# Performance work log

Measured on AMD Instinct MI355X. Metric: run time of the kernel, lower is better.

The kernel has to match this reference:

```python
import jax, jax.numpy as jnp
import numpy as np

SCALE = 2
PAD = 4
EPS = 1e-5
K = 5
N, C, H, W = 4, 64, 128, 128


def _splits(a, s):
    # (..., W, H) -> (..., W/s, H/s, s*s), block decimation matching torch view/permute
    *lead, Wd, Hd = a.shape
    b = a.reshape(*lead, s, Wd // s, s, Hd // s)
    nl = len(lead)
    b = jnp.transpose(b, tuple(range(nl)) + (nl + 1, nl + 3, nl, nl + 2))
    return b.reshape(*lead, Wd // s, Hd // s, s * s)


def _p2o(psf, Hs, Ws):
    # PSF -> OTF: zero-pad, roll to center at origin, FFT
    kh, kw = psf.shape[-2], psf.shape[-1]
    otf = jnp.zeros(psf.shape[:-2] + (Hs, Ws), psf.dtype).at[..., :kh, :kw].set(psf)
    otf = jnp.roll(otf, (-(kh // 2), -(kw // 2)), axis=(-2, -1))
    return jnp.fft.fftn(otf, axes=(-2, -1))


def _upsample(x, s):
    # s-fold zero-filling upsampler (S^T y)
    n, c, h, w = x.shape
    return jnp.zeros((n, c, h * s, w * s), x.dtype).at[..., ::s, ::s].set(x)


def setup_inputs() -> dict:
    key = jax.random.key(0)
    kx, kw_, _ = jax.random.split(key, 3)
    x = jax.random.normal(kx, (N, C, H, W), dtype=jnp.float32)
    w_raw = jax.random.normal(kw_, (1, C, K, K), dtype=jnp.float32)
    weight = jax.nn.softmax(w_raw.reshape(1, C, -1), axis=-1).reshape(1, C, K, K)
    bias = jnp.zeros((1, C, 1, 1), dtype=jnp.float32)
    return {"x": x, "weight": weight, "bias": bias}


def reference(x, weight, bias):
    s = SCALE
    xp = jnp.pad(x, ((0, 0), (0, 0), (PAD, PAD), (PAD, PAD)), mode="wrap")  # circular
    biaseps = jax.nn.sigmoid(bias - 9.0) + EPS  # (1,C,1,1)
    _, _, h, w = xp.shape
    STy = _upsample(xp, s)  # zero-filled upsample
    # nearest-neighbor interpolate by integer factor s
    xn = jnp.repeat(jnp.repeat(xp, s, axis=-2), s, axis=-1)
    FB = _p2o(weight, h * s, w * s)           # (1,C,hs,ws) complex
    FBC = jnp.conj(FB)
    F2B = jnp.abs(FB) ** 2                     # real
    FBFy = FBC * jnp.fft.fftn(STy, axes=(-2, -1))
    FR = FBFy + jnp.fft.fftn(biaseps * xn, axes=(-2, -1))
    x1 = FB * FR
    FBR = jnp.mean(_splits(x1, s), axis=-1)    # (N,C,h,w) complex
    invW = jnp.mean(_splits(F2B, s), axis=-1)  # (1,C,h,w) real
    invWBR = FBR / (invW + biaseps)
    FCBinvWBR = FBC * jnp.tile(invWBR, (1, 1, s, s))
    FX = (FR - FCBinvWBR) / biaseps
    out = jnp.real(jnp.fft.ifftn(FX, axes=(-2, -1)))
    out = out[..., PAD * s:-PAD * s, PAD * s:-PAD * s]
    return out
```

## Files before the change

### kernel.cpp

```cpp
#include <hip/hip_runtime.h>
#include <math.h>


#define MDIM 136
#define RSC  70
#define HC   69
#define PLANE_HALF (MDIM*HC)
#define NPLANES 256
#define LDS_CPLX (MDIM*RSC + MDIM)
#define PI_D 3.14159265358979323846

__device__ __forceinline__ int slot136(int k) { return 17*(k & 7) + (k >> 3); }
__device__ __forceinline__ int slot68(int k)  { return 17*(k & 3) + (k >> 2); }

template<int DIR>
__device__ __forceinline__ void dft17(float2* __restrict__ z, int base, int stride)
{
    constexpr float C17[9] = {1.f, 0.93247223f, 0.73900892f, 0.44573836f,
                              0.09226836f, -0.27366299f, -0.60263464f,
                              -0.85021714f, -0.98297310f};
    constexpr float S17[9] = {0.f, 0.36124167f, 0.67369564f, 0.89516329f,
                              0.99573418f, 0.96182564f, 0.79801723f,
                              0.52643216f, 0.18374952f};
    constexpr float d = (DIR > 0) ? 1.f : -1.f;
    float xr[17], xi[17];
#pragma unroll
    for (int n = 0; n < 17; n++) {
        float2 v = z[base + n*stride];
        xr[n] = v.x; xi[n] = v.y;
    }
    float ar[8], ai[8], br[8], bi[8];
#pragma unroll
    for (int n = 1; n <= 8; n++) {
        ar[n-1] = xr[n] + xr[17-n];  ai[n-1] = xi[n] + xi[17-n];
        br[n-1] = xr[n] - xr[17-n];  bi[n-1] = xi[n] - xi[17-n];
    }
    float s0r = xr[0], s0i = xi[0];
#pragma unroll
    for (int n = 0; n < 8; n++) { s0r += ar[n]; s0i += ai[n]; }
    z[base] = make_float2(s0r, s0i);
#pragma unroll
    for (int k = 1; k <= 8; k++) {
        float Pr = xr[0], Pi = xi[0], Qr = 0.f, Qi = 0.f;
#pragma unroll
        for (int n = 1; n <= 8; n++) {
            int m = (k*n) % 17;
            float cc = (m <= 8) ? C17[m] : C17[17-m];
            float ss = (m <= 8) ? S17[m] : -S17[17-m];
            Pr = fmaf(ar[n-1], cc, Pr);
            Pi = fmaf(ai[n-1], cc, Pi);
            Qr = fmaf(br[n-1], ss, Qr);
            Qi = fmaf(bi[n-1], ss, Qi);
        }
        z[base + k*stride]      = make_float2(Pr - d*Qi, Pi + d*Qr);
        z[base + (17-k)*stride] = make_float2(Pr + d*Qi, Pi - d*Qr);
    }
}

template<int DIR>
__device__ void fft136_cols(float2* __restrict__ z, const float2* __restrict__ lut,
                            int ncols, int tid, int nth)
{
    constexpr float d = (DIR > 0) ? 1.0f : -1.0f;
    constexpr float C707 = 0.70710678118654752f;
    for (int e = tid; e < ncols*17; e += nth) {
        int c  = e / 17;
        int n2 = e - c*17;
        float xr[8], xi[8];
#pragma unroll
        for (int n1 = 0; n1 < 8; n1++) {
            float2 v = z[(17*n1 + n2)*RSC + c];
            xr[n1] = v.x; xi[n1] = v.y;
        }
        float e0r = xr[0]+xr[4], e0i = xi[0]+xi[4];
        float e1r = xr[0]-xr[4], e1i = xi[0]-xi[4];
        float o0r = xr[2]+xr[6], o0i = xi[2]+xi[6];
        float o1r = xr[2]-xr[6], o1i = xi[2]-xi[6];
        float E0r = e0r+o0r, E0i = e0i+o0i;
        float E2r = e0r-o0r, E2i = e0i-o0i;
        float E1r = e1r - d*o1i, E1i = e1i + d*o1r;
        float E3r = e1r + d*o1i, E3i = e1i - d*o1r;
        float f0r = xr[1]+xr[5], f0i = xi[1]+xi[5];
        float f1r = xr[1]-xr[5], f1i = xi[1]-xi[5];
        float h0r = xr[3]+xr[7], h0i = xi[3]+xi[7];
        float h1r = xr[3]-xr[7], h1i = xi[3]-xi[7];
        float O0r = f0r+h0r, O0i = f0i+h0i;
        float O2r = f0r-h0r, O2i = f0i-h0i;
        float O1r = f1r - d*h1i, O1i = f1i + d*h1r;
        float O3r = f1r + d*h1i, O3i = f1i - d*h1r;
        float t1r =  C707*(O1r - d*O1i), t1i = C707*(O1i + d*O1r);
        float t2r = -d*O2i,              t2i = d*O2r;
        float t3r = -C707*(O3r + d*O3i), t3i = C707*(d*O3r - O3i);
        float Xr[8], Xi[8];
        Xr[0]=E0r+O0r; Xi[0]=E0i+O0i;  Xr[4]=E0r-O0r; Xi[4]=E0i-O0i;
        Xr[1]=E1r+t1r; Xi[1]=E1i+t1i;  Xr[5]=E1r-t1r; Xi[5]=E1i-t1i;
        Xr[2]=E2r+t2r; Xi[2]=E2i+t2i;  Xr[6]=E2r-t2r; Xi[6]=E2i-t2i;
        Xr[3]=E3r+t3r; Xi[3]=E3i+t3i;  Xr[7]=E3r-t3r; Xi[7]=E3i-t3i;
        float2 w = lut[n2];
        float wr = w.x, wi = w.y;
        float cr = 1.f, ci = 0.f;
#pragma unroll
        for (int k1 = 0; k1 < 8; k1++) {
            int a = (17*k1 + n2)*RSC + c;
            z[a] = make_float2(Xr[k1]*cr - Xi[k1]*ci, Xr[k1]*ci + Xi[k1]*cr);
            float ncr = cr*wr - ci*wi;
            ci = cr*wi + ci*wr; cr = ncr;
        }
    }
    __syncthreads();
    for (int e = tid; e < ncols*8; e += nth) {
        int c  = e >> 3;
        int k1 = e & 7;
        dft17<DIR>(z, 17*k1*RSC + c, RSC);
    }
    __syncthreads();
}

template<int DIR>
__device__ void ct68_rows(float2* __restrict__ z, const float2* __restrict__ lut,
                          int tid, int nth)
{
    constexpr float d = (DIR > 0) ? 1.0f : -1.0f;
    for (int e = tid; e < MDIM*17; e += nth) {
        int row = e / 17;
        int n2  = e - row*17;
        int base = row*RSC;
        float xr[4], xi[4];
#pragma unroll
        for (int n1 = 0; n1 < 4; n1++) {
            float2 v = z[base + 17*n1 + n2];
            xr[n1] = v.x; xi[n1] = v.y;
        }
        float t0r = xr[0]+xr[2], t0i = xi[0]+xi[2];
        float t1r = xr[0]-xr[2], t1i = xi[0]-xi[2];
        float t2r = xr[1]+xr[3], t2i = xi[1]+xi[3];
        float t3r = xr[1]-xr[3], t3i = xi[1]-xi[3];
        float Xr[4], Xi[4];
        Xr[0] = t0r+t2r;      Xi[0] = t0i+t2i;
        Xr[2] = t0r-t2r;      Xi[2] = t0i-t2i;
        Xr[1] = t1r - d*t3i;  Xi[1] = t1i + d*t3r;
        Xr[3] = t1r + d*t3i;  Xi[3] = t1i - d*t3r;
        float2 w = lut[2*n2];
        float wr = w.x, wi = w.y;
        float cr = 1.f, ci = 0.f;
#pragma unroll
        for (int k1 = 0; k1 < 4; k1++) {
            int a = base + 17*k1 + n2;
            z[a] = make_float2(Xr[k1]*cr - Xi[k1]*ci, Xr[k1]*ci + Xi[k1]*cr);
            float ncr = cr*wr - ci*wi;
            ci = cr*wi + ci*wr; cr = ncr;
        }
    }
    __syncthreads();
    for (int e = tid; e < MDIM*4; e += nth) {
        int row = e >> 2;
        int k1  = e & 3;
        dft17<DIR>(z, row*RSC + 17*k1, 1);
    }
    __syncthreads();
}

__global__ __launch_bounds__(1024, 8) void fwd_kernel(const float* __restrict__ x,
                                                      float2* __restrict__ Xhat)
{
    extern __shared__ float2 zsm[];
    float2* z   = zsm;
    float2* lut = zsm + MDIM*RSC;
    const int tid = threadIdx.x, nth = blockDim.x;

    for (int t = tid; t < MDIM; t += nth) {
        double s, c; sincos(-2.0*PI_D*(double)t/136.0, &s, &c);
        lut[t] = make_float2((float)c, (float)s);
    }
    const float* xp = x + (size_t)blockIdx.x * (128*128);
    for (int e = tid; e < MDIM*68; e += nth) {
        int i = e / 68, n = e - i*68;
        int si = (i + 124) & 127;
        int j0 = (2*n + 124) & 127;
        z[i*RSC + n] = *reinterpret_cast<const float2*>(xp + si*128 + j0);
    }
    __syncthreads();
    ct68_rows<-1>(z, lut, tid, nth);
    for (int e = tid; e < MDIM*35; e += nth) {
        int row = e / 35, k = e - row*35;
        int base = row*RSC;
        int sa = slot68(k);
        float2 Za = z[base+sa];
        float Zar = Za.x, Zai = Za.y;
        float Zbr, Zbi; int sb;
        if (k == 0) { Zbr = Zar; Zbi = Zai; sb = 68; }
        else {
            int kk = 68-k; sb = slot68(kk);
            float2 Zb = z[base+sb]; Zbr = Zb.x; Zbi = Zb.y;
        }
        float2 w = lut[k];
        float wc = w.x, ws = w.y;
        float Er = 0.5f*(Zar + Zbr), Ei = 0.5f*(Zai - Zbi);
        float Dr = 0.5f*(Zar - Zbr), Di = 0.5f*(Zai + Zbi);
        float Tr = wc*Dr - ws*Di, Ti = wc*Di + ws*Dr;
        z[base+sa] = make_float2(Er + Ti, Ei - Tr);
        float E2r = Er,  E2i = -Ei;
        float D2r = -Dr, D2i = Di;
        float w2c = -wc, w2s = ws;
        float T2r = w2c*D2r - w2s*D2i, T2i = w2c*D2i + w2s*D2r;
        z[base+sb] = make_float2(E2r + T2i, E2i - T2r);
    }
    __syncthreads();
    fft136_cols<-1>(z, lut, HC, tid, nth);
    float2* outp = Xhat + (size_t)blockIdx.x * PLANE_HALF;
    for (int e = tid; e < PLANE_HALF; e += nth) {
        int g1 = e / HC, g2 = e - g1*HC;
        int cq = (g2 == 68) ? 68 : slot68(g2);
        outp[e] = z[slot136(g1)*RSC + cq];
    }
}

__global__ void prep_kernel(const float* __restrict__ weight,
                            const float* __restrict__ bias,
                            float2* __restrict__ Abuf)
{
    __shared__ double tabc[272], tabs[272];
    for (int t = threadIdx.x; t < 272; t += blockDim.x) {
        double s, c; sincos(-2.0*PI_D*(double)t/272.0, &s, &c);
        tabc[t] = c; tabs[t] = s;
    }
    __syncthreads();

    const int c     = blockIdx.x >> 3;
    const int chunk = blockIdx.x & 7;
    const float* wp = weight + c*25;
    double w[25];
#pragma unroll
    for (int i = 0; i < 25; i++) w[i] = (double)wp[i];
    const double r = 1.0/(1.0 + exp(9.0 - (double)bias[c])) + 1e-5;

    const int e_lo = chunk * 1173;
    const int e_hi = e_lo + 1173;
    for (int e = e_lo + (int)threadIdx.x; e < e_hi; e += blockDim.x) {
        int g1 = e / HC, g2 = e - g1*HC;
        double c1 = tabc[g1], s1 = tabs[g1];
        double c2 = tabc[g2], s2 = tabs[g2];
        double e1r[5], e1i[5], e2r[5], e2i[5];
        e1r[2]=1.0; e1i[2]=0.0; e1r[3]=c1; e1i[3]=s1;
        e1r[4]=c1*c1-s1*s1; e1i[4]=2.0*c1*s1;
        e1r[1]=c1; e1i[1]=-s1; e1r[0]=e1r[4]; e1i[0]=-e1i[4];
        e2r[2]=1.0; e2i[2]=0.0; e2r[3]=c2; e2i[3]=s2;
        e2r[4]=c2*c2-s2*s2; e2i[4]=2.0*c2*s2;
        e2r[1]=c2; e2i[1]=-s2; e2r[0]=e2r[4]; e2i[0]=-e2i[4];

        double R0r[5],R0i[5],R1r[5],R1i[5];
#pragma unroll
        for (int a = 0; a < 5; a++) {
            double r0r=0,r0i=0,r1r=0,r1i=0;
#pragma unroll
            for (int b = 0; b < 5; b++) {
                double wv = w[a*5+b];
                double pr = wv*e2r[b], pi = wv*e2i[b];
                r0r += pr; r0i += pi;
                if (b & 1) { r1r -= pr; r1i -= pi; } else { r1r += pr; r1i += pi; }
            }
            R0r[a]=r0r; R0i[a]=r0i; R1r[a]=r1r; R1i[a]=r1i;
        }
        double FBr[2][2], FBi[2][2];
#pragma unroll
        for (int a1 = 0; a1 < 2; a1++)
#pragma unroll
            for (int b1 = 0; b1 < 2; b1++) {
                double fr=0, fi=0;
#pragma unroll
                for (int a = 0; a < 5; a++) {
                    double er = e1r[a], ei = e1i[a];
                    if (a1 && (a & 1)) { er = -er; ei = -ei; }
                    double Rr = b1 ? R1r[a] : R0r[a];
                    double Ri = b1 ? R1i[a] : R0i[a];
                    fr += er*Rr - ei*Ri;
                    fi += er*Ri + ei*Rr;
                }
                FBr[a1][b1]=fr; FBi[a1][b1]=fi;
            }
        double ur[2]={1.0+c1, 1.0-c1}, ui[2]={s1, -s1};
        double vr[2]={1.0+c2, 1.0-c2}, vi[2]={s2, -s2};
        double Br_[2][2], Bi_[2][2];
#pragma unroll
        for (int a1 = 0; a1 < 2; a1++)
#pragma unroll
            for (int b1 = 0; b1 < 2; b1++) {
                Br_[a1][b1] = ur[a1]*vr[b1] - ui[a1]*vi[b1];
                Bi_[a1][b1] = ur[a1]*vi[b1] + ui[a1]*vr[b1];
            }
        double invW=0, Qr=0, Qi=0;
#pragma unroll
        for (int a1 = 0; a1 < 2; a1++)
#pragma unroll
            for (int b1 = 0; b1 < 2; b1++) {
                invW += FBr[a1][b1]*FBr[a1][b1] + FBi[a1][b1]*FBi[a1][b1];
                Qr += FBr[a1][b1]*Br_[a1][b1] - FBi[a1][b1]*Bi_[a1][b1];
                Qi += FBr[a1][b1]*Bi_[a1][b1] + FBi[a1][b1]*Br_[a1][b1];
            }
        invW *= 0.25; Qr *= 0.25; Qi *= 0.25;
        double den = 1.0/(invW + r);
        double Sr = (1.0 - Qr)*den, Si = -Qi*den;
        double Mr[2][2], Mi[2][2];
#pragma unroll
        for (int a1 = 0; a1 < 2; a1++)
#pragma unroll
            for (int b1 = 0; b1 < 2; b1++) {
                Mr[a1][b1] = Br_[a1][b1] + FBr[a1][b1]*Sr + FBi[a1][b1]*Si;
                Mi[a1][b1] = Bi_[a1][b1] + FBr[a1][b1]*Si - FBi[a1][b1]*Sr;
            }
        const double scale = 1.0/73984.0;
#pragma unroll
        for (int uu = 0; uu < 2; uu++)
#pragma unroll
            for (int vv = 0; vv < 2; vv++) {
                double sr=0, si=0;
#pragma unroll
                for (int a1 = 0; a1 < 2; a1++)
#pragma unroll
                    for (int b1 = 0; b1 < 2; b1++) {
                        if ((a1*uu + b1*vv) & 1) { sr -= Mr[a1][b1]; si -= Mi[a1][b1]; }
                        else                     { sr += Mr[a1][b1]; si += Mi[a1][b1]; }
                    }
                int t = g1*uu + g2*vv;
                double pc = tabc[t], ps = -tabs[t];
                float2 outv;
                outv.x = (float)((pc*sr - ps*si)*scale);
                outv.y = (float)((pc*si + ps*sr)*scale);
                Abuf[((size_t)(c*4 + uu*2 + vv))*PLANE_HALF + e] = outv;
            }
    }
}

__global__ __launch_bounds__(1024, 8) void inv_kernel(const float2* __restrict__ Xhat,
                                                      const float2* __restrict__ Abuf,
                                                      float* __restrict__ out)
{
    extern __shared__ float2 zsm[];
    float2* z   = zsm;
    float2* lut = zsm + MDIM*RSC;
    const int tid = threadIdx.x, nth = blockDim.x;

    for (int t = tid; t < MDIM; t += nth) {
        double s, c; sincos(2.0*PI_D*(double)t/136.0, &s, &c);
        lut[t] = make_float2((float)c, (float)s);
    }
    const int p  = blockIdx.x;
    const int u  = p & 1;
    const int v  = (p >> 3) & 1;
    const int nc = ((p >> 4) << 2) | ((p >> 1) & 3);
    const int c  = nc & 63;
    const float2* Xp = Xhat + (size_t)nc * PLANE_HALF;
    const float2* Ap = Abuf + (size_t)(c*4 + u*2 + v) * PLANE_HALF;

    for (int e = tid; e < PLANE_HALF; e += nth) {
        int g1 = e / HC, g2 = e - g1*HC;
        float2 xv = Xp[e], av = Ap[e];
        z[g1*RSC + g2] = make_float2(av.x*xv.x - av.y*xv.y,
                                     av.x*xv.y + av.y*xv.x);
    }
    __syncthreads();
    fft136_cols<1>(z, lut, HC, tid, nth);
    for (int e = tid; e < MDIM*35; e += nth) {
        int row = e / 35, k = e - row*35;
        int base = row*RSC;
        float2 Ta = z[base+k];
        float2 Tb = z[base+68-k];
        float Tar = Ta.x, Tai = Ta.y;
        float Tbr = Tb.x, Tbi = Tb.y;
        float Sr = Tar + Tbr, Si = Tai - Tbi;
        float Dr = Tar - Tbr, Di = Tai + Tbi;
        float2 w = lut[k];
        float wc = w.x, ws = w.y;
        float Or = wc*Dr - ws*Di, Oi = wc*Di + ws*Dr;
        z[base+k] = make_float2(Sr - Oi, Si + Or);
        if (k >= 1 && k <= 33) {
            float S2r = Tbr + Tar, S2i = Tbi - Tai;
            float D2r = Tbr - Tar, D2i = Tbi + Tai;
            float w2c = -wc, w2s = ws;
            float O2r = w2c*D2r - w2s*D2i, O2i = w2c*D2i + w2s*D2r;
            z[base+68-k] = make_float2(S2r - O2i, S2i + O2r);
        }
    }
    __syncthreads();
    ct68_rows<1>(z, lut, tid, nth);
    float* op = out + (size_t)nc * (256*256);
    for (int e = tid; e < 128*64; e += nth) {
        int y1 = 4 + (e >> 6);
        int m  = 2 + (e & 63);
        float2 wv = z[slot136(y1)*RSC + slot68(m)];
        int o1 = 2*y1 + u - 8;
        op[o1*256 + 4*m + v - 8] = wv.x;
        op[o1*256 + 4*m + v - 6] = wv.y;
    }
}

extern "C" void kernel_launch(void* const* d_in, const int* in_sizes, int n_in,
                              void* d_out, int out_size, void* d_ws, size_t ws_size,
                              hipStream_t stream)
{
    const float* x      = (const float*)d_in[0];
    const float* weight = (const float*)d_in[1];
    const float* bias   = (const float*)d_in[2];
    float* out = (float*)d_out;

    float2* Xhat = (float2*)d_ws;
    float2* Abuf = Xhat + (size_t)NPLANES * PLANE_HALF;

    const size_t lds_bytes = (size_t)LDS_CPLX * sizeof(float2);
    (void)hipFuncSetAttribute((const void*)fwd_kernel,
                              hipFuncAttributeMaxDynamicSharedMemorySize, (int)lds_bytes);
    (void)hipFuncSetAttribute((const void*)inv_kernel,
                              hipFuncAttributeMaxDynamicSharedMemorySize, (int)lds_bytes);

    prep_kernel<<<512, 256, 0, stream>>>(weight, bias, Abuf);
    fwd_kernel<<<NPLANES, 1024, lds_bytes, stream>>>(x, Xhat);
    inv_kernel<<<NPLANES*4, 1024, lds_bytes, stream>>>(Xhat, Abuf, out);
}
```

Baseline: 151.2 us.

## Fuse final DFT17 stages with global stores and merge c2r pack into radix-4 pass

The final radix-17 DFT pass of each FFT now writes its outputs straight to global memory, with the index permutation built in. This removes a shared-memory round trip, a barrier and the separate gather/scatter loop. In the inverse kernel, the complex-to-real untangling step is merged with the first radix-4 row stage. The change also strength-reduces index math (no divides inside loops, using a fixed 1024 threads), reads twiddles from the LUT directly instead of recurrence multiplies, and computes the LUT with float sincosf instead of double. The global stores become strided or scattered, which may hurt coalescing, and float twiddles reduce accuracy slightly.

Measured after the change: 166.8 us. +10.4%, slower.

```diff
diff --git a/kernel.cpp b/kernel.cpp
--- a/kernel.cpp
+++ b/kernel.cpp
@@ -9,12 +9,12 @@
 #define NPLANES 256
 #define LDS_CPLX (MDIM*RSC + MDIM)
 #define PI_D 3.14159265358979323846
-
-__device__ __forceinline__ int slot136(int k) { return 17*(k & 7) + (k >> 3); }
+#define NTH 1024
+
 __device__ __forceinline__ int slot68(int k)  { return 17*(k & 3) + (k >> 2); }
 
-template<int DIR>
-__device__ __forceinline__ void dft17(float2* __restrict__ z, int base, int stride)
+template<int DIR, class F>
+__device__ __forceinline__ void dft17_sink(float2* z, int base, int stride, F f)
 {
     constexpr float C17[9] = {1.f, 0.93247223f, 0.73900892f, 0.44573836f,
                               0.09226836f, -0.27366299f, -0.60263464f,
@@ -38,7 +38,7 @@
     float s0r = xr[0], s0i = xi[0];
 #pragma unroll
     for (int n = 0; n < 8; n++) { s0r += ar[n]; s0i += ai[n]; }
-    z[base] = make_float2(s0r, s0i);
+    f(0, s0r, s0i);
 #pragma unroll
     for (int k = 1; k <= 8; k++) {
         float Pr = xr[0], Pi = xi[0], Qr = 0.f, Qi = 0.f;
@@ -52,20 +52,39 @@
             Qr = fmaf(br[n-1], ss, Qr);
             Qi = fmaf(bi[n-1], ss, Qi);
         }
-        z[base + k*stride]      = make_float2(Pr - d*Qi, Pi + d*Qr);
-        z[base + (17-k)*stride] = make_float2(Pr + d*Qi, Pi - d*Qr);
+        f(k,    Pr - d*Qi, Pi + d*Qr);
+        f(17-k, Pr + d*Qi, Pi - d*Qr);
     }
 }
 
 template<int DIR>
-__device__ void fft136_cols(float2* __restrict__ z, const float2* __restrict__ lut,
-                            int ncols, int tid, int nth)
+__device__ __forceinline__ void radix4_tw(float2* z, const float2* lut, int base, int n2,
+                                          float2 Z0, float2 Z1, float2 Z2, float2 Z3)
+{
+    constexpr float d = (DIR > 0) ? 1.0f : -1.0f;
+    float t0r = Z0.x+Z2.x, t0i = Z0.y+Z2.y;
+    float t1r = Z0.x-Z2.x, t1i = Z0.y-Z2.y;
+    float t2r = Z1.x+Z3.x, t2i = Z1.y+Z3.y;
+    float t3r = Z1.x-Z3.x, t3i = Z1.y-Z3.y;
+    float X0r = t0r+t2r,     X0i = t0i+t2i;
+    float X2r = t0r-t2r,     X2i = t0i-t2i;
+    float X1r = t1r - d*t3i, X1i = t1i + d*t3r;
+    float X3r = t1r + d*t3i, X3i = t1i - d*t3r;
+    z[base + n2] = make_float2(X0r, X0i);
+    float2 w1 = lut[2*n2], w2 = lut[4*n2], w3 = lut[6*n2];
+    z[base + 17 + n2] = make_float2(X1r*w1.x - X1i*w1.y, X1r*w1.y + X1i*w1.x);
+    z[base + 34 + n2] = make_float2(X2r*w2.x - X2i*w2.y, X2r*w2.y + X2i*w2.x);
+    z[base + 51 + n2] = make_float2(X3r*w3.x - X3i*w3.y, X3r*w3.y + X3i*w3.x);
+}
+
+template<int DIR>
+__device__ void fft136_s1(float2* z, const float2* lut, int ncols, int tid)
 {
     constexpr float d = (DIR > 0) ? 1.0f : -1.0f;
     constexpr float C707 = 0.70710678118654752f;
-    for (int e = tid; e < ncols*17; e += nth) {
-        int c  = e / 17;
-        int n2 = e - c*17;
+    int c = tid / 17;
+    int n2 = tid - c*17;
+    for (int e = tid; e < ncols*17; e += NTH) {
         float xr[8], xi[8];
 #pragma unroll
         for (int n1 = 0; n1 < 8; n1++) {
@@ -96,68 +115,41 @@
         Xr[1]=E1r+t1r; Xi[1]=E1i+t1i;  Xr[5]=E1r-t1r; Xi[5]=E1i-t1i;
         Xr[2]=E2r+t2r; Xi[2]=E2i+t2i;  Xr[6]=E2r-t2r; Xi[6]=E2i-t2i;
         Xr[3]=E3r+t3r; Xi[3]=E3i+t3i;  Xr[7]=E3r-t3r; Xi[7]=E3i-t3i;
-        float2 w = lut[n2];
-        float wr = w.x, wi = w.y;
-        float cr = 1.f, ci = 0.f;
-#pragma unroll
-        for (int k1 = 0; k1 < 8; k1++) {
-            int a = (17*k1 + n2)*RSC + c;
-            z[a] = make_float2(Xr[k1]*cr - Xi[k1]*ci, Xr[k1]*ci + Xi[k1]*cr);
-            float ncr = cr*wr - ci*wi;
-            ci = cr*wi + ci*wr; cr = ncr;
-        }
-    }
-    __syncthreads();
-    for (int e = tid; e < ncols*8; e += nth) {
-        int c  = e >> 3;
-        int k1 = e & 7;
-        dft17<DIR>(z, 17*k1*RSC + c, RSC);
-    }
-    __syncthreads();
+        z[n2*RSC + c] = make_float2(Xr[0], Xi[0]);
+        int ti = 0;
+#pragma unroll
+        for (int k1 = 1; k1 < 8; k1++) {
+            ti += n2;
+            float2 w = lut[ti];
+            z[(17*k1 + n2)*RSC + c] = make_float2(Xr[k1]*w.x - Xi[k1]*w.y,
+                                                  Xr[k1]*w.y + Xi[k1]*w.x);
+        }
+        c += 60; n2 += 4; if (n2 >= 17) { n2 -= 17; c++; }
+    }
 }
 
 template<int DIR>
-__device__ void ct68_rows(float2* __restrict__ z, const float2* __restrict__ lut,
-                          int tid, int nth)
-{
-    constexpr float d = (DIR > 0) ? 1.0f : -1.0f;
-    for (int e = tid; e < MDIM*17; e += nth) {
-        int row = e / 17;
-        int n2  = e - row*17;
+__device__ void ct68_s1(float2* z, const float2* lut, int tid)
+{
+    int row = tid / 17;
+    int n2  = tid - row*17;
+    for (int e = tid; e < MDIM*17; e += NTH) {
         int base = row*RSC;
-        float xr[4], xi[4];
-#pragma unroll
-        for (int n1 = 0; n1 < 4; n1++) {
-            float2 v = z[base + 17*n1 + n2];
-            xr[n1] = v.x; xi[n1] = v.y;
-        }
-        float t0r = xr[0]+xr[2], t0i = xi[0]+xi[2];
-        float t1r = xr[0]-xr[2], t1i = xi[0]-xi[2];
-        float t2r = xr[1]+xr[3], t2i = xi[1]+xi[3];
-        float t3r = xr[1]-xr[3], t3i = xi[1]-xi[3];
-        float Xr[4], Xi[4];
-        Xr[0] = t0r+t2r;      Xi[0] = t0i+t2i;
-        Xr[2] = t0r-t2r;      Xi[2] = t0i-t2i;
-        Xr[1] = t1r - d*t3i;  Xi[1] = t1i + d*t3r;
-        Xr[3] = t1r + d*t3i;  Xi[3] = t1i - d*t3r;
-        float2 w = lut[2*n2];
-        float wr = w.x, wi = w.y;
-        float cr = 1.f, ci = 0.f;
-#pragma unroll
-        for (int k1 = 0; k1 < 4; k1++) {
-            int a = base + 17*k1 + n2;
-            z[a] = make_float2(Xr[k1]*cr - Xi[k1]*ci, Xr[k1]*ci + Xi[k1]*cr);
-            float ncr = cr*wr - ci*wi;
-            ci = cr*wi + ci*wr; cr = ncr;
-        }
-    }
-    __syncthreads();
-    for (int e = tid; e < MDIM*4; e += nth) {
-        int row = e >> 2;
-        int k1  = e & 3;
-        dft17<DIR>(z, row*RSC + 17*k1, 1);
-    }
-    __syncthreads();
+        float2 Z0 = z[base + n2];
+        float2 Z1 = z[base + 17 + n2];
+        float2 Z2 = z[base + 34 + n2];
+        float2 Z3 = z[base + 51 + n2];
+        radix4_tw<DIR>(z, lut, base, n2, Z0, Z1, Z2, Z3);
+        row += 60; n2 += 4; if (n2 >= 17) { n2 -= 17; row++; }
+    }
+}
+
+__device__ __forceinline__ float2 c2r_pack(float2 a, float2 b, float2 w)
+{
+    float Sr = a.x + b.x, Si = a.y - b.y;
+    float Dr = a.x - b.x, Di = a.y + b.y;
+    float Or = w.x*Dr - w.y*Di, Oi = w.x*Di + w.y*Dr;
+    return make_float2(Sr - Oi, Si + Or);
 }
 
 __global__ __launch_bounds__(1024, 8) void fwd_kernel(const float* __restrict__ x,
@@ -166,52 +158,73 @@
     extern __shared__ float2 zsm[];
     float2* z   = zsm;
     float2* lut = zsm + MDIM*RSC;
-    const int tid = threadIdx.x, nth = blockDim.x;
-
-    for (int t = tid; t < MDIM; t += nth) {
-        double s, c; sincos(-2.0*PI_D*(double)t/136.0, &s, &c);
-        lut[t] = make_float2((float)c, (float)s);
+    const int tid = threadIdx.x;
+
+    if (tid < MDIM) {
+        float s, c; sincosf(-2.0f*(float)PI_D*(float)tid/136.0f, &s, &c);
+        lut[tid] = make_float2(c, s);
     }
     const float* xp = x + (size_t)blockIdx.x * (128*128);
-    for (int e = tid; e < MDIM*68; e += nth) {
-        int i = e / 68, n = e - i*68;
-        int si = (i + 124) & 127;
-        int j0 = (2*n + 124) & 127;
-        z[i*RSC + n] = *reinterpret_cast<const float2*>(xp + si*128 + j0);
-    }
-    __syncthreads();
-    ct68_rows<-1>(z, lut, tid, nth);
-    for (int e = tid; e < MDIM*35; e += nth) {
-        int row = e / 35, k = e - row*35;
-        int base = row*RSC;
-        int sa = slot68(k);
-        float2 Za = z[base+sa];
-        float Zar = Za.x, Zai = Za.y;
-        float Zbr, Zbi; int sb;
-        if (k == 0) { Zbr = Zar; Zbi = Zai; sb = 68; }
-        else {
-            int kk = 68-k; sb = slot68(kk);
-            float2 Zb = z[base+sb]; Zbr = Zb.x; Zbi = Zb.y;
-        }
-        float2 w = lut[k];
-        float wc = w.x, ws = w.y;
-        float Er = 0.5f*(Zar + Zbr), Ei = 0.5f*(Zai - Zbi);
-        float Dr = 0.5f*(Zar - Zbr), Di = 0.5f*(Zai + Zbi);
-        float Tr = wc*Dr - ws*Di, Ti = wc*Di + ws*Dr;
-        z[base+sa] = make_float2(Er + Ti, Ei - Tr);
-        float E2r = Er,  E2i = -Ei;
-        float D2r = -Dr, D2i = Di;
-        float w2c = -wc, w2s = ws;
-        float T2r = w2c*D2r - w2s*D2i, T2i = w2c*D2i + w2s*D2r;
-        z[base+sb] = make_float2(E2r + T2i, E2i - T2r);
-    }
-    __syncthreads();
-    fft136_cols<-1>(z, lut, HC, tid, nth);
+    {
+        int i = tid / 68, n = tid - (tid/68)*68;
+        for (int e = tid; e < MDIM*68; e += NTH) {
+            int si = (i + 124) & 127;
+            int j0 = (2*n + 124) & 127;
+            z[i*RSC + n] = *reinterpret_cast<const float2*>(xp + si*128 + j0);
+            i += 15; n += 4; if (n >= 68) { n -= 68; i++; }
+        }
+    }
+    __syncthreads();
+    ct68_s1<-1>(z, lut, tid);
+    __syncthreads();
+    if (tid < MDIM*4) {
+        int row = tid >> 2, k1 = tid & 3;
+        int base = row*RSC + 17*k1;
+        dft17_sink<-1>(z, base, 1, [&](int k2, float re, float im) {
+            z[base + k2] = make_float2(re, im);
+        });
+    }
+    __syncthreads();
+    {
+        int row = tid / 35, k = tid - (tid/35)*35;
+        for (int e = tid; e < MDIM*35; e += NTH) {
+            int base = row*RSC;
+            int sa = slot68(k);
+            float2 Za = z[base+sa];
+            float Zar = Za.x, Zai = Za.y;
+            float Zbr, Zbi; int sb;
+            if (k == 0) { Zbr = Zar; Zbi = Zai; sb = 68; }
+            else {
+                int kk = 68-k; sb = slot68(kk);
+                float2 Zb = z[base+sb]; Zbr = Zb.x; Zbi = Zb.y;
+            }
+            float2 w = lut[k];
+            float wc = w.x, ws = w.y;
+            float Er = 0.5f*(Zar + Zbr), Ei = 0.5f*(Zai - Zbi);
+            float Dr = 0.5f*(Zar - Zbr), Di = 0.5f*(Zai + Zbi);
+            float Tr = wc*Dr - ws*Di, Ti = wc*Di + ws*Dr;
+            z[base+sa] = make_float2(Er + Ti, Ei - Tr);
+            float E2r = Er,  E2i = -Ei;
+            float D2r = -Dr, D2i = Di;
+            float w2c = -wc, w2s = ws;
+            float T2r = w2c*D2r - w2s*D2i, T2i = w2c*D2i + w2s*D2r;
+            z[base+sb] = make_float2(E2r + T2i, E2i - T2r);
+            row += 29; k += 9; if (k >= 35) { k -= 35; row++; }
+        }
+    }
+    __syncthreads();
+    fft136_s1<-1>(z, lut, HC, tid);
+    __syncthreads();
     float2* outp = Xhat + (size_t)blockIdx.x * PLANE_HALF;
-    for (int e = tid; e < PLANE_HALF; e += nth) {
-        int g1 = e / HC, g2 = e - g1*HC;
-        int cq = (g2 == 68) ? 68 : slot68(g2);
-        outp[e] = z[slot136(g1)*RSC + cq];
+    if (tid < HC*8) {
+        int c = tid >> 3, k1 = tid & 7;
+        int cd = (c*241) >> 12;
+        int cm = c - 17*cd;
+        int g2 = (c == 68) ? 68 : (4*cm + cd);
+        float2* op2 = outp + g2;
+        dft17_sink<-1>(z, 17*k1*RSC + c, RSC, [&](int k2, float re, float im) {
+            op2[(size_t)(k1 + 8*k2)*HC] = make_float2(re, im);
+        });
     }
 }
 
@@ -338,11 +351,11 @@
     extern __shared__ float2 zsm[];
     float2* z   = zsm;
     float2* lut = zsm + MDIM*RSC;
-    const int tid = threadIdx.x, nth = blockDim.x;
-
-    for (int t = tid; t < MDIM; t += nth) {
-        double s, c; sincos(2.0*PI_D*(double)t/136.0, &s, &c);
-        lut[t] = make_float2((float)c, (float)s);
+    const int tid = threadIdx.x;
+
+    if (tid < MDIM) {
+        float s, c; sincosf(2.0f*(float)PI_D*(float)tid/136.0f, &s, &c);
+        lut[tid] = make_float2(c, s);
     }
     const int p  = blockIdx.x;
     const int u  = p & 1;
@@ -352,45 +365,75 @@
     const float2* Xp = Xhat + (size_t)nc * PLANE_HALF;
     const float2* Ap = Abuf + (size_t)(c*4 + u*2 + v) * PLANE_HALF;
 
-    for (int e = tid; e < PLANE_HALF; e += nth) {
-        int g1 = e / HC, g2 = e - g1*HC;
-        float2 xv = Xp[e], av = Ap[e];
-        z[g1*RSC + g2] = make_float2(av.x*xv.x - av.y*xv.y,
-                                     av.x*xv.y + av.y*xv.x);
-    }
-    __syncthreads();
-    fft136_cols<1>(z, lut, HC, tid, nth);
-    for (int e = tid; e < MDIM*35; e += nth) {
-        int row = e / 35, k = e - row*35;
-        int base = row*RSC;
-        float2 Ta = z[base+k];
-        float2 Tb = z[base+68-k];
-        float Tar = Ta.x, Tai = Ta.y;
-        float Tbr = Tb.x, Tbi = Tb.y;
-        float Sr = Tar + Tbr, Si = Tai - Tbi;
-        float Dr = Tar - Tbr, Di = Tai + Tbi;
-        float2 w = lut[k];
-        float wc = w.x, ws = w.y;
-        float Or = wc*Dr - ws*Di, Oi = wc*Di + ws*Dr;
-        z[base+k] = make_float2(Sr - Oi, Si + Or);
-        if (k >= 1 && k <= 33) {
-            float S2r = Tbr + Tar, S2i = Tbi - Tai;
-            float D2r = Tbr - Tar, D2i = Tbi + Tai;
-            float w2c = -wc, w2s = ws;
-            float O2r = w2c*D2r - w2s*D2i, O2i = w2c*D2i + w2s*D2r;
-            z[base+68-k] = make_float2(S2r - O2i, S2i + O2r);
-        }
-    }
-    __syncthreads();
-    ct68_rows<1>(z, lut, tid, nth);
+    {
+        int g1 = tid / HC, g2 = tid - (tid/HC)*HC;
+        for (int e = tid; e < PLANE_HALF; e += NTH) {
+            float2 xv = Xp[e], av = Ap[e];
+            z[g1*RSC + g2] = make_float2(av.x*xv.x - av.y*xv.y,
+                                         av.x*xv.y + av.y*xv.x);
+            g1 += 14; g2 += 58; if (g2 >= HC) { g2 -= HC; g1++; }
+        }
+    }
+    __syncthreads();
+    fft136_s1<1>(z, lut, HC, tid);
+    __syncthreads();
+    if (tid < HC*8) {
+        int cc = tid >> 3, k1 = tid & 7;
+        int base = 17*k1*RSC + cc;
+        dft17_sink<1>(z, base, RSC, [&](int k2, float re, float im) {
+            z[base + k2*RSC] = make_float2(re, im);
+        });
+    }
+    __syncthreads();
+    {
+        int row = tid / 9, g = tid - (tid/9)*9;
+        for (int e = tid; e < MDIM*9; e += NTH) {
+            int base = row*RSC;
+            if (g == 0) {
+                float2 T0  = z[base],    T17 = z[base+17], T34 = z[base+34],
+                       T51 = z[base+51], T68 = z[base+68];
+                float2 Z0 = c2r_pack(T0,  T68, lut[0]);
+                float2 Z1 = c2r_pack(T17, T51, lut[17]);
+                float2 Z2 = c2r_pack(T34, T34, lut[34]);
+                float2 Z3 = c2r_pack(T51, T17, lut[51]);
+                radix4_tw<1>(z, lut, base, 0, Z0, Z1, Z2, Z3);
+            } else {
+                int gb = 17 - g;
+                float2 Ta0 = z[base+g],    Ta1 = z[base+g+17],
+                       Ta2 = z[base+g+34], Ta3 = z[base+g+51];
+                float2 Tb0 = z[base+gb],    Tb1 = z[base+gb+17],
+                       Tb2 = z[base+gb+34], Tb3 = z[base+gb+51];
+                float2 Za0 = c2r_pack(Ta0, Tb3, lut[g]);
+                float2 Za1 = c2r_pack(Ta1, Tb2, lut[g+17]);
+                float2 Za2 = c2r_pack(Ta2, Tb1, lut[g+34]);
+                float2 Za3 = c2r_pack(Ta3, Tb0, lut[g+51]);
+                float2 Zb0 = c2r_pack(Tb0, Ta3, lut[gb]);
+                float2 Zb1 = c2r_pack(Tb1, Ta2, lut[gb+17]);
+                float2 Zb2 = c2r_pack(Tb2, Ta1, lut[gb+34]);
+                float2 Zb3 = c2r_pack(Tb3, Ta0, lut[gb+51]);
+                radix4_tw<1>(z, lut, base, g,  Za0, Za1, Za2, Za3);
+                radix4_tw<1>(z, lut, base, gb, Zb0, Zb1, Zb2, Zb3);
+            }
+            row += 113; g += 7; if (g >= 9) { g -= 9; row++; }
+        }
+    }
+    __syncthreads();
     float* op = out + (size_t)nc * (256*256);
-    for (int e = tid; e < 128*64; e += nth) {
-        int y1 = 4 + (e >> 6);
-        int m  = 2 + (e & 63);
-        float2 wv = z[slot136(y1)*RSC + slot68(m)];
-        int o1 = 2*y1 + u - 8;
-        op[o1*256 + 4*m + v - 8] = wv.x;
-        op[o1*256 + 4*m + v - 6] = wv.y;
+    if (tid < MDIM*4) {
+        int row = tid >> 2, k1 = tid & 3;
+        int rq = (row*241) >> 12;
+        int rm = row - 17*rq;
+        int y1 = 8*rm + rq;
+        if (y1 >= 4 && y1 < 132) {
+            float* rowp = op + (size_t)(2*y1 + u - 8)*256 + v - 8;
+            dft17_sink<1>(z, row*RSC + 17*k1, 1, [&](int k2, float re, float im) {
+                int m = k1 + 4*k2;
+                if (m >= 2 && m < 66) {
+                    rowp[4*m]     = re;
+                    rowp[4*m + 2] = im;
+                }
+            });
+        }
     }
 }
 
```
